# Kernel tuning notes

Hardware: AMD Instinct MI355X
Metric: run time of the kernel (lower is better)

The kernel has to match this reference:

```python
import jax, jax.numpy as jnp
import numpy as np
import math

B, N, D, H = 32, 577, 768, 12
HD = D // H  # 64
WS = 24  # window size
NUM_REL_DIST = (2 * WS - 1) * (2 * WS - 1) + 3  # 2212


def _build_rel_pos_index():
    ch, cw = np.arange(WS), np.arange(WS)
    coords = np.stack(np.meshgrid(ch, cw, indexing='ij'))  # [2, WS, WS]
    cf = coords.reshape(2, -1)  # [2, WS*WS]
    rel = cf[:, :, None] - cf[:, None, :]  # [2, WS*WS, WS*WS]
    rel = rel.transpose(1, 2, 0).astype(np.int64)
    rel[:, :, 0] += WS - 1
    rel[:, :, 1] += WS - 1
    rel[:, :, 0] *= 2 * WS - 1
    idx = np.zeros((WS * WS + 1, WS * WS + 1), dtype=np.int64)
    idx[1:, 1:] = rel.sum(-1)
    idx[0, 0:] = NUM_REL_DIST - 3
    idx[0:, 0] = NUM_REL_DIST - 2
    idx[0, 0] = NUM_REL_DIST - 1
    return idx.astype(np.int32)


def setup_inputs() -> dict:
    key = jax.random.key(0)
    ks = jax.random.split(key, 7)
    s = 1.0 / math.sqrt(D)
    return {
        'hidden_states': jax.random.normal(ks[0], (B, N, D), jnp.float32),
        'q_w': jax.random.normal(ks[1], (D, D), jnp.float32) * s,
        'q_b': jax.random.normal(ks[2], (D,), jnp.float32) * 0.02,
        'k_w': jax.random.normal(ks[3], (D, D), jnp.float32) * s,
        'v_w': jax.random.normal(ks[4], (D, D), jnp.float32) * s,
        'v_b': jax.random.normal(ks[5], (D,), jnp.float32) * 0.02,
        'rel_pos_table': jax.random.normal(ks[6], (NUM_REL_DIST, H), jnp.float32) * 0.02,
        'rel_pos_index': jnp.asarray(_build_rel_pos_index()),
    }


def reference(hidden_states, q_w, q_b, k_w, v_w, v_b, rel_pos_table, rel_pos_index):
    # QKV projections (torch Linear: x @ W.T + b); key has no bias
    q = hidden_states @ q_w.T + q_b  # [B,N,D]
    k = hidden_states @ k_w.T        # [B,N,D]
    v = hidden_states @ v_w.T + v_b  # [B,N,D]

    def heads(x):
        return x.reshape(B, N, H, HD).transpose(0, 2, 1, 3)  # [B,H,N,HD]

    q, k, v = heads(q), heads(k), heads(v)
    scores = jnp.einsum('bhqd,bhkd->bhqk', q, k) / math.sqrt(HD)
    # relative position bias: table lookup -> [N,N,H] -> [H,N,N]
    bias = rel_pos_table[rel_pos_index.reshape(-1)].reshape(N, N, H)
    scores = scores + bias.transpose(2, 0, 1)[None]
    probs = jax.nn.softmax(scores, axis=-1)  # dropout p=0 (eval)
    ctx = jnp.einsum('bhqk,bhkd->bhqd', probs, v)
    return ctx.transpose(0, 2, 1, 3).reshape(B, N, D)
```

## Files before the change

kernel.cpp:

```cpp
#include <hip/hip_runtime.h>
#include <hip/hip_bf16.h>

#define B_  32
#define N_  577
#define D_  768
#define H_  12
#define HD_ 64
#define M_  (B_ * N_)
#define NW_ (3 * D_)
#define VN_ 640
#define BPAD_ 640
#define SCALE_ 0.18033688f

typedef __bf16 bf16_t;
typedef __bf16 bf16x8 __attribute__((ext_vector_type(8)));
typedef __bf16 bf16x4 __attribute__((ext_vector_type(4)));
typedef float  f32x4  __attribute__((ext_vector_type(4)));

static __device__ __forceinline__ bf16x8 ldg8(const bf16_t* p) {
    return *reinterpret_cast<const bf16x8*>(p);
}

#define GLOAD_LDS16(g, l)                                                     \
    __builtin_amdgcn_global_load_lds(                                         \
        (const __attribute__((address_space(1))) void*)(g),                   \
        (__attribute__((address_space(3))) void*)(l), 16, 0, 0)

__global__ void cvt_f32_bf16(const float* __restrict__ src,
                             bf16_t* __restrict__ dst, int n4) {
    int i = blockIdx.x * blockDim.x + threadIdx.x;
    if (i < n4) {
        float4 f = reinterpret_cast<const float4*>(src)[i];
        bf16x4 o;
        o.x = (bf16_t)f.x; o.y = (bf16_t)f.y; o.z = (bf16_t)f.z; o.w = (bf16_t)f.w;
        *reinterpret_cast<bf16x4*>(dst + (size_t)i * 4) = o;
    }
}

__global__ void cvt3_f32_bf16(const float* __restrict__ s0,
                              const float* __restrict__ s1,
                              const float* __restrict__ s2,
                              bf16_t* __restrict__ dst, int n4) {
    int i = blockIdx.x * blockDim.x + threadIdx.x;
    if (i < n4) {
        const float* src = blockIdx.y == 0 ? s0 : (blockIdx.y == 1 ? s1 : s2);
        float4 f = reinterpret_cast<const float4*>(src)[i];
        bf16x4 o;
        o.x = (bf16_t)f.x; o.y = (bf16_t)f.y; o.z = (bf16_t)f.z; o.w = (bf16_t)f.w;
        *reinterpret_cast<bf16x4*>(dst + (size_t)blockIdx.y * n4 * 4 + (size_t)i * 4) = o;
    }
}

__global__ void build_bias_t(const float* __restrict__ table,
                             const int* __restrict__ idx,
                             float* __restrict__ biasT) {
    int col = blockIdx.x;
    int h   = blockIdx.y;
    float* dst = biasT + ((size_t)h * BPAD_ + col) * BPAD_;
    if (col < N_) {
        for (int row = threadIdx.x; row < BPAD_; row += blockDim.x) {
            int rr = row < N_ ? row : (N_ - 1);
            int id = idx[rr * N_ + col];
            dst[row] = table[id * H_ + h] * 1.44269504f;
        }
    } else {
        for (int row = threadIdx.x; row < BPAD_; row += blockDim.x)
            dst[row] = -1e30f;
    }
}

__global__ __launch_bounds__(256) void qkv_gemm(
    const bf16_t* __restrict__ hb, const bf16_t* __restrict__ W,
    const float* __restrict__ qb, const float* __restrict__ vb,
    bf16_t* __restrict__ Q, bf16_t* __restrict__ K, bf16_t* __restrict__ VT)
{
    __shared__ __align__(16) char lds[65536];

    int tid = threadIdx.x;
    int w  = tid >> 6, l = tid & 63;
    int lr = l & 15, lg = l >> 4;
    int wm = w & 1,  wn = w >> 1;

    int wg = blockIdx.x;
    int xcd = wg & 7, pos = wg >> 3;
    const int Q8 = 2610 / 8, R8 = 2610 % 8;
    int base = xcd < R8 ? xcd * (Q8 + 1) : R8 * (Q8 + 1) + (xcd - R8) * Q8;
    int wgid = base + pos;
    int bx = wgid / 18, y = wgid - bx * 18;
    int brow = bx * 128;
    int mat = y / 6, ysub = y - mat * 6;
    int cbase = ysub * 128;

    int srow = tid >> 3;
    int sslot = (tid & 7) ^ (srow & 7);
    const bf16_t* pa[4];
    const bf16_t* pb[4];
#pragma unroll
    for (int r = 0; r < 4; ++r) {
        int ra = brow + r * 32 + srow; ra = ra < M_ ? ra : (M_ - 1);
        pa[r] = hb + (size_t)ra * D_ + sslot * 8;
        pb[r] = W + (size_t)(y * 128 + r * 32 + srow) * D_ + sslot * 8;
    }

    auto stage = [&](int buf, int k) {
#pragma unroll
        for (int r = 0; r < 4; ++r) {
            GLOAD_LDS16(pa[r] + k, lds + buf * 16384 + r * 4096 + tid * 16);
            GLOAD_LDS16(pb[r] + k, lds + 32768 + buf * 16384 + r * 4096 + tid * 16);
        }
    };

    f32x4 acc[4][4] = {};
    stage(0, 0);
    int cur = 0;
    for (int t = 0; t < 12; ++t) {
        if (t < 11) {
            stage(cur ^ 1, (t + 1) * 64);
            asm volatile("s_waitcnt vmcnt(8)" ::: "memory");
        } else {
            asm volatile("s_waitcnt vmcnt(0)" ::: "memory");
        }
        __builtin_amdgcn_s_barrier();
        __builtin_amdgcn_sched_barrier(0);

        const char* pA = lds + cur * 16384;
        const char* pB = lds + 32768 + cur * 16384;
#pragma unroll
        for (int kk = 0; kk < 2; ++kk) {
            bf16x8 af[4];
#pragma unroll
            for (int m = 0; m < 4; ++m) {
                int row = wm * 64 + m * 16 + lr;
                af[m] = *reinterpret_cast<const bf16x8*>(
                    pA + row * 128 + (((kk * 4 + lg) ^ (lr & 7)) << 4));
            }
#pragma unroll
            for (int n = 0; n < 4; ++n) {
                int row = wn * 64 + n * 16 + lr;
                bf16x8 bfr = *reinterpret_cast<const bf16x8*>(
                    pB + row * 128 + (((kk * 4 + lg) ^ (lr & 7)) << 4));
#pragma unroll
                for (int m = 0; m < 4; ++m)
                    acc[m][n] = __builtin_amdgcn_mfma_f32_16x16x32_bf16(
                        af[m], bfr, acc[m][n], 0, 0, 0);
            }
        }
        __builtin_amdgcn_sched_barrier(0);
        __builtin_amdgcn_s_barrier();
        cur ^= 1;
    }

    bf16_t* ep = (bf16_t*)lds;
    if (mat < 2) {
#pragma unroll
        for (int m = 0; m < 4; ++m)
#pragma unroll
            for (int n = 0; n < 4; ++n) {
                int col = wn * 64 + n * 16 + lr;
#pragma unroll
                for (int j = 0; j < 4; ++j) {
                    int row = wm * 64 + m * 16 + lg * 4 + j;
                    float v = acc[m][n][j];
                    v = (mat == 0) ? (v + qb[cbase + col]) * SCALE_ : v;
                    ep[row * 132 + col] = (bf16_t)v;
                }
            }
        __syncthreads();
        bf16_t* dst0 = (mat == 0) ? Q : K;
#pragma unroll
        for (int k = 0; k < 8; ++k) {
            int c = k * 256 + tid;
            int row = c >> 4, cc = c & 15;
            int grow = brow + row;
            if (grow < M_) {
                int bb = grow / N_, nn = grow - bb * N_;
                int col0 = cc * 8;
                int hh = ysub * 2 + (col0 >> 6);
                int hd0 = col0 & 63;
                bf16x8 vc = *reinterpret_cast<const bf16x8*>(ep + row * 132 + col0);
                *reinterpret_cast<bf16x8*>(
                    dst0 + ((size_t)(bb * H_ + hh) * N_ + nn) * HD_ + hd0) = vc;
            }
        }
    } else {
#pragma unroll
        for (int m = 0; m < 4; ++m)
#pragma unroll
            for (int n = 0; n < 4; ++n) {
                int col = wn * 64 + n * 16 + lr;
                float badd = vb[cbase + col];
#pragma unroll
                for (int j = 0; j < 4; ++j) {
                    int row = wm * 64 + m * 16 + lg * 4 + j;
                    ep[col * 132 + row] = (bf16_t)(acc[m][n][j] + badd);
                }
            }
        __syncthreads();
#pragma unroll
        for (int k = 0; k < 8; ++k) {
            int c = k * 256 + tid;
            int col = c >> 4, rc = c & 15;
            int grow0 = brow + rc * 8;
            int hh = ysub * 2 + (col >> 6), hd = col & 63;
            int bb = grow0 / N_, nn0 = grow0 - bb * N_;
            if (nn0 + 8 <= N_ && grow0 + 8 <= M_) {
                *reinterpret_cast<bf16x8*>(
                    VT + ((size_t)(bb * H_ + hh) * HD_ + hd) * VN_ + nn0) =
                    *reinterpret_cast<const bf16x8*>(ep + col * 132 + rc * 8);
            } else {
                for (int jj = 0; jj < 8; ++jj) {
                    int grow = grow0 + jj;
                    if (grow >= M_) break;
                    int b2 = grow / N_, n2 = grow - b2 * N_;
                    VT[((size_t)(b2 * H_ + hh) * HD_ + hd) * VN_ + n2] =
                        ep[col * 132 + rc * 8 + jj];
                }
            }
        }
    }
}

__global__ __launch_bounds__(256) void attn(
    const bf16_t* __restrict__ Q, const bf16_t* __restrict__ K,
    const bf16_t* __restrict__ VT, const float* __restrict__ biasT,
    float* __restrict__ out)
{
    __shared__ __align__(16) char Kl[2][8192];
    __shared__ __align__(16) char Vl[2][8192];
    __shared__ __align__(16) char Pl[4][2048];

    int tid = threadIdx.x;
    int w = tid >> 6, l = tid & 63, lr = l & 15, lg = l >> 4;

    int wg = blockIdx.x;
    int wgid = (wg & 7) * 480 + (wg >> 3);
    int h = wgid / 320;
    int rem = wgid - h * 320;
    int b = rem / 10;
    int qt = rem - b * 10;

    const bf16_t* Qp = Q  + (size_t)(b * H_ + h) * N_ * HD_;
    const bf16_t* Kp = K  + (size_t)(b * H_ + h) * N_ * HD_;
    const bf16_t* Vp = VT + (size_t)(b * H_ + h) * HD_ * VN_;
    const float*  bp = biasT + (size_t)h * BPAD_ * BPAD_;

    int q0 = qt * 64 + w * 16;
    int qrow = q0 + lr;
    int qrow_c = qrow < N_ ? qrow : (N_ - 1);
    bf16x8 aQ0 = ldg8(Qp + (size_t)qrow_c * HD_ + lg * 8);
    bf16x8 aQ1 = ldg8(Qp + (size_t)qrow_c * HD_ + 32 + lg * 8);

    bf16x8 vone;
#pragma unroll
    for (int i = 0; i < 8; ++i) vone[i] = (bf16_t)1.0f;

    int rloc = l >> 3;
    int cswz = (l & 7) ^ rloc;
    const bf16_t* Kst[2];
    const bf16_t* Vst[2];
#pragma unroll
    for (int rnd = 0; rnd < 2; ++rnd) {
        int r = rnd * 32 + w * 8 + rloc;
        Kst[rnd] = Kp + (size_t)r * HD_ + cswz * 8;
        Vst[rnd] = Vp + (size_t)r * VN_ + cswz * 8;
    }

    f32x4 o[4] = {};
    f32x4 osum = {};
    char* Pw = Pl[w];
    const int NT = 10;

    auto stageKV = [&](int buf, int k0) {
#pragma unroll
        for (int rnd = 0; rnd < 2; ++rnd)
            GLOAD_LDS16(Kst[rnd] + (size_t)k0 * HD_,
                        Kl[buf] + rnd * 4096 + w * 1024);
#pragma unroll
        for (int rnd = 0; rnd < 2; ++rnd)
            GLOAD_LDS16(Vst[rnd] + k0, Vl[buf] + rnd * 4096 + w * 1024);
    };
    auto loadBias = [&](int k0, f32x4* bbv) {
#pragma unroll
        for (int kt = 0; kt < 4; ++kt)
            bbv[kt] = *reinterpret_cast<const f32x4*>(
                bp + (size_t)(k0 + kt * 16 + lr) * BPAD_ + q0 + lg * 4);
    };

    auto tile = [&](int t, int rbuf, const f32x4* bbcur, f32x4* bbnxt) {
        int k0 = t * 64;
        if (t + 1 < NT) {
            stageKV(rbuf ^ 1, k0 + 64);
            loadBias(k0 + 64, bbnxt);
        }
        __builtin_amdgcn_sched_barrier(0);

        f32x4 s[4];
        __builtin_amdgcn_s_setprio(1);
#pragma unroll
        for (int kt = 0; kt < 4; ++kt) {
            int r = kt * 16 + lr;
            bf16x8 kf0 = *reinterpret_cast<const bf16x8*>(
                Kl[rbuf] + r * 128 + ((lg ^ (r & 7)) << 4));
            bf16x8 kf1 = *reinterpret_cast<const bf16x8*>(
                Kl[rbuf] + r * 128 + (((4 + lg) ^ (r & 7)) << 4));
            f32x4 a = __builtin_amdgcn_mfma_f32_16x16x32_bf16(
                aQ0, kf0, bbcur[kt], 0, 0, 0);
            s[kt] = __builtin_amdgcn_mfma_f32_16x16x32_bf16(aQ1, kf1, a, 0, 0, 0);
        }
        __builtin_amdgcn_s_setprio(0);

#pragma unroll
        for (int kt = 0; kt < 4; ++kt)
#pragma unroll
            for (int j = 0; j < 4; ++j) {
                float p = __builtin_amdgcn_exp2f(s[kt][j]);
                int row = lg * 4 + j;
                int byte = (row * 128 + (kt * 16 + lr) * 2) ^ ((row & 7) << 4);
                *reinterpret_cast<bf16_t*>(Pw + byte) = (bf16_t)p;
            }

        __builtin_amdgcn_s_setprio(1);
#pragma unroll
        for (int kc = 0; kc < 2; ++kc) {
            int pbyte = (lr * 128 + kc * 64 + lg * 16) ^ ((lr & 7) << 4);
            bf16x8 aP = *reinterpret_cast<const bf16x8*>(Pw + pbyte);
            osum = __builtin_amdgcn_mfma_f32_16x16x32_bf16(aP, vone, osum, 0, 0, 0);
#pragma unroll
            for (int ft = 0; ft < 4; ++ft) {
                int d = ft * 16 + lr;
                bf16x8 bV = *reinterpret_cast<const bf16x8*>(
                    Vl[rbuf] + d * 128 + (((kc * 4 + lg) ^ (d & 7)) << 4));
                o[ft] = __builtin_amdgcn_mfma_f32_16x16x32_bf16(aP, bV, o[ft], 0, 0, 0);
            }
        }
        __builtin_amdgcn_s_setprio(0);
        __builtin_amdgcn_sched_barrier(0);

        if (t + 1 < NT) asm volatile("s_waitcnt vmcnt(4)" ::: "memory");
        else            asm volatile("s_waitcnt vmcnt(0)" ::: "memory");
        __builtin_amdgcn_s_barrier();
        __builtin_amdgcn_sched_barrier(0);
    };

    f32x4 bbA[4], bbB[4];
    stageKV(0, 0);
    loadBias(0, bbA);
    asm volatile("s_waitcnt vmcnt(4)" ::: "memory");
    __builtin_amdgcn_s_barrier();
    __builtin_amdgcn_sched_barrier(0);

    for (int tp = 0; tp < NT / 2; ++tp) {
        tile(tp * 2,     0, bbA, bbB);
        tile(tp * 2 + 1, 1, bbB, bbA);
    }

#pragma unroll
    for (int j = 0; j < 4; ++j) {
        int row = q0 + lg * 4 + j;
        if (row < N_) {
            float inv = 1.f / osum[j];
#pragma unroll
            for (int ft = 0; ft < 4; ++ft)
                out[((size_t)(b * N_ + row)) * D_ + h * HD_ + ft * 16 + lr] =
                    o[ft][j] * inv;
        }
    }
}

extern "C" void kernel_launch(void* const* d_in, const int* in_sizes, int n_in,
                              void* d_out, int out_size, void* d_ws, size_t ws_size,
                              hipStream_t stream)
{
    const float* hs    = (const float*)d_in[0];
    const float* q_w   = (const float*)d_in[1];
    const float* q_b   = (const float*)d_in[2];
    const float* k_w   = (const float*)d_in[3];
    const float* v_w   = (const float*)d_in[4];
    const float* v_b   = (const float*)d_in[5];
    const float* table = (const float*)d_in[6];
    const int*   rpi   = (const int*)d_in[7];
    float* out = (float*)d_out;

    char* ws = (char*)d_ws;
    size_t off = 0;
    auto alloc = [&](size_t bytes) {
        char* p = ws + off;
        off = (off + bytes + 255) & ~(size_t)255;
        return p;
    };
    bf16_t* hb  = (bf16_t*)alloc((size_t)M_ * D_ * 2);
    bf16_t* Wc  = (bf16_t*)alloc((size_t)NW_ * D_ * 2);
    bf16_t* Qb  = (bf16_t*)alloc((size_t)B_ * H_ * N_ * HD_ * 2);
    bf16_t* Kb  = (bf16_t*)alloc((size_t)B_ * H_ * N_ * HD_ * 2 + 16384);
    bf16_t* VTb = (bf16_t*)alloc((size_t)B_ * H_ * HD_ * VN_ * 2);
    float*  bia = (float*)alloc((size_t)H_ * BPAD_ * BPAD_ * 4);

    int n4h = M_ * D_ / 4;
    cvt_f32_bf16<<<(n4h + 255) / 256, 256, 0, stream>>>(hs, hb, n4h);
    int n4w = D_ * D_ / 4;
    cvt3_f32_bf16<<<dim3((n4w + 255) / 256, 3), 256, 0, stream>>>(
        q_w, k_w, v_w, Wc, n4w);
    build_bias_t<<<dim3(BPAD_, H_), 256, 0, stream>>>(table, rpi, bia);

    qkv_gemm<<<2610, 256, 0, stream>>>(hb, Wc, q_b, v_b, Qb, Kb, VTb);

    attn<<<3840, 256, 0, stream>>>(Qb, Kb, VTb, bia, out);
}
```

Before: 238.4 us.

## Process two 64-query tiles per attention workgroup to reuse staged K/V

Each attention workgroup now computes 128 query rows (two 16-row sub-tiles per wave) against the same K/V tiles staged in LDS, halving the grid size. This is meant to halve K/V global loads and LDS staging per query and give each wave more independent MFMA work. In exchange it doubles accumulator and bias registers per thread, which may reduce occupancy, and leaves fewer workgroups to balance across CUs.

```diff
diff --git a/kernel.cpp b/kernel.cpp
--- a/kernel.cpp
+++ b/kernel.cpp
@@ -227,28 +227,34 @@
 {
     __shared__ __align__(16) char Kl[2][8192];
     __shared__ __align__(16) char Vl[2][8192];
-    __shared__ __align__(16) char Pl[4][2048];
+    __shared__ __align__(16) char Pl[4][2][2048];
 
     int tid = threadIdx.x;
     int w = tid >> 6, l = tid & 63, lr = l & 15, lg = l >> 4;
 
     int wg = blockIdx.x;
-    int wgid = (wg & 7) * 480 + (wg >> 3);
-    int h = wgid / 320;
-    int rem = wgid - h * 320;
-    int b = rem / 10;
-    int qt = rem - b * 10;
+    int wgid = (wg & 7) * 240 + (wg >> 3);
+    int h = wgid / 160;
+    int rem = wgid - h * 160;
+    int b = rem / 5;
+    int qt = rem - b * 5;
 
     const bf16_t* Qp = Q  + (size_t)(b * H_ + h) * N_ * HD_;
     const bf16_t* Kp = K  + (size_t)(b * H_ + h) * N_ * HD_;
     const bf16_t* Vp = VT + (size_t)(b * H_ + h) * HD_ * VN_;
     const float*  bp = biasT + (size_t)h * BPAD_ * BPAD_;
 
-    int q0 = qt * 64 + w * 16;
-    int qrow = q0 + lr;
-    int qrow_c = qrow < N_ ? qrow : (N_ - 1);
-    bf16x8 aQ0 = ldg8(Qp + (size_t)qrow_c * HD_ + lg * 8);
-    bf16x8 aQ1 = ldg8(Qp + (size_t)qrow_c * HD_ + 32 + lg * 8);
+    int q0A = qt * 128 + w * 16;
+    int q0B = q0A + 64;
+    bf16x8 aQ0A, aQ1A, aQ0B, aQ1B;
+    {
+        int qa = q0A + lr; qa = qa < N_ ? qa : (N_ - 1);
+        int qb2 = q0B + lr; qb2 = qb2 < N_ ? qb2 : (N_ - 1);
+        aQ0A = ldg8(Qp + (size_t)qa * HD_ + lg * 8);
+        aQ1A = ldg8(Qp + (size_t)qa * HD_ + 32 + lg * 8);
+        aQ0B = ldg8(Qp + (size_t)qb2 * HD_ + lg * 8);
+        aQ1B = ldg8(Qp + (size_t)qb2 * HD_ + 32 + lg * 8);
+    }
 
     bf16x8 vone;
 #pragma unroll
@@ -265,9 +271,10 @@
         Vst[rnd] = Vp + (size_t)r * VN_ + cswz * 8;
     }
 
-    f32x4 o[4] = {};
-    f32x4 osum = {};
-    char* Pw = Pl[w];
+    f32x4 oA[4] = {}, oB[4] = {};
+    f32x4 osumA = {}, osumB = {};
+    char* PwA = Pl[w][0];
+    char* PwB = Pl[w][1];
     const int NT = 10;
 
     auto stageKV = [&](int buf, int k0) {
@@ -279,22 +286,25 @@
         for (int rnd = 0; rnd < 2; ++rnd)
             GLOAD_LDS16(Vst[rnd] + k0, Vl[buf] + rnd * 4096 + w * 1024);
     };
-    auto loadBias = [&](int k0, f32x4* bbv) {
-#pragma unroll
-        for (int kt = 0; kt < 4; ++kt)
-            bbv[kt] = *reinterpret_cast<const f32x4*>(
-                bp + (size_t)(k0 + kt * 16 + lr) * BPAD_ + q0 + lg * 4);
+    auto loadBias = [&](int k0, f32x4* bA, f32x4* bB) {
+#pragma unroll
+        for (int kt = 0; kt < 4; ++kt) {
+            const float* bcol = bp + (size_t)(k0 + kt * 16 + lr) * BPAD_;
+            bA[kt] = *reinterpret_cast<const f32x4*>(bcol + q0A + lg * 4);
+            bB[kt] = *reinterpret_cast<const f32x4*>(bcol + q0B + lg * 4);
+        }
     };
 
-    auto tile = [&](int t, int rbuf, const f32x4* bbcur, f32x4* bbnxt) {
+    auto tile = [&](int t, int rbuf, const f32x4* bcA, const f32x4* bcB,
+                    f32x4* bnA, f32x4* bnB) {
         int k0 = t * 64;
         if (t + 1 < NT) {
             stageKV(rbuf ^ 1, k0 + 64);
-            loadBias(k0 + 64, bbnxt);
+            loadBias(k0 + 64, bnA, bnB);
         }
         __builtin_amdgcn_sched_barrier(0);
 
-        f32x4 s[4];
+        f32x4 sA[4], sB[4];
         __builtin_amdgcn_s_setprio(1);
 #pragma unroll
         for (int kt = 0; kt < 4; ++kt) {
@@ -303,9 +313,12 @@
                 Kl[rbuf] + r * 128 + ((lg ^ (r & 7)) << 4));
             bf16x8 kf1 = *reinterpret_cast<const bf16x8*>(
                 Kl[rbuf] + r * 128 + (((4 + lg) ^ (r & 7)) << 4));
-            f32x4 a = __builtin_amdgcn_mfma_f32_16x16x32_bf16(
-                aQ0, kf0, bbcur[kt], 0, 0, 0);
-            s[kt] = __builtin_amdgcn_mfma_f32_16x16x32_bf16(aQ1, kf1, a, 0, 0, 0);
+            f32x4 a0 = __builtin_amdgcn_mfma_f32_16x16x32_bf16(
+                aQ0A, kf0, bcA[kt], 0, 0, 0);
+            sA[kt] = __builtin_amdgcn_mfma_f32_16x16x32_bf16(aQ1A, kf1, a0, 0, 0, 0);
+            f32x4 a1 = __builtin_amdgcn_mfma_f32_16x16x32_bf16(
+                aQ0B, kf0, bcB[kt], 0, 0, 0);
+            sB[kt] = __builtin_amdgcn_mfma_f32_16x16x32_bf16(aQ1B, kf1, a1, 0, 0, 0);
         }
         __builtin_amdgcn_s_setprio(0);
 
@@ -313,56 +326,69 @@
         for (int kt = 0; kt < 4; ++kt)
 #pragma unroll
             for (int j = 0; j < 4; ++j) {
-                float p = __builtin_amdgcn_exp2f(s[kt][j]);
                 int row = lg * 4 + j;
                 int byte = (row * 128 + (kt * 16 + lr) * 2) ^ ((row & 7) << 4);
-                *reinterpret_cast<bf16_t*>(Pw + byte) = (bf16_t)p;
+                *reinterpret_cast<bf16_t*>(PwA + byte) =
+                    (bf16_t)__builtin_amdgcn_exp2f(sA[kt][j]);
+                *reinterpret_cast<bf16_t*>(PwB + byte) =
+                    (bf16_t)__builtin_amdgcn_exp2f(sB[kt][j]);
             }
 
         __builtin_amdgcn_s_setprio(1);
 #pragma unroll
         for (int kc = 0; kc < 2; ++kc) {
             int pbyte = (lr * 128 + kc * 64 + lg * 16) ^ ((lr & 7) << 4);
-            bf16x8 aP = *reinterpret_cast<const bf16x8*>(Pw + pbyte);
-            osum = __builtin_amdgcn_mfma_f32_16x16x32_bf16(aP, vone, osum, 0, 0, 0);
+            bf16x8 aPA = *reinterpret_cast<const bf16x8*>(PwA + pbyte);
+            bf16x8 aPB = *reinterpret_cast<const bf16x8*>(PwB + pbyte);
+            osumA = __builtin_amdgcn_mfma_f32_16x16x32_bf16(aPA, vone, osumA, 0, 0, 0);
+            osumB = __builtin_amdgcn_mfma_f32_16x16x32_bf16(aPB, vone, osumB, 0, 0, 0);
 #pragma unroll
             for (int ft = 0; ft < 4; ++ft) {
                 int d = ft * 16 + lr;
                 bf16x8 bV = *reinterpret_cast<const bf16x8*>(
                     Vl[rbuf] + d * 128 + (((kc * 4 + lg) ^ (d & 7)) << 4));
-                o[ft] = __builtin_amdgcn_mfma_f32_16x16x32_bf16(aP, bV, o[ft], 0, 0, 0);
+                oA[ft] = __builtin_amdgcn_mfma_f32_16x16x32_bf16(aPA, bV, oA[ft], 0, 0, 0);
+                oB[ft] = __builtin_amdgcn_mfma_f32_16x16x32_bf16(aPB, bV, oB[ft], 0, 0, 0);
             }
         }
         __builtin_amdgcn_s_setprio(0);
         __builtin_amdgcn_sched_barrier(0);
 
-        if (t + 1 < NT) asm volatile("s_waitcnt vmcnt(4)" ::: "memory");
+        if (t + 1 < NT) asm volatile("s_waitcnt vmcnt(8)" ::: "memory");
         else            asm volatile("s_waitcnt vmcnt(0)" ::: "memory");
         __builtin_amdgcn_s_barrier();
         __builtin_amdgcn_sched_barrier(0);
     };
 
-    f32x4 bbA[4], bbB[4];
+    f32x4 bbA0[4], bbB0[4], bbA1[4], bbB1[4];
     stageKV(0, 0);
-    loadBias(0, bbA);
-    asm volatile("s_waitcnt vmcnt(4)" ::: "memory");
+    loadBias(0, bbA0, bbB0);
+    asm volatile("s_waitcnt vmcnt(8)" ::: "memory");
     __builtin_amdgcn_s_barrier();
     __builtin_amdgcn_sched_barrier(0);
 
     for (int tp = 0; tp < NT / 2; ++tp) {
-        tile(tp * 2,     0, bbA, bbB);
-        tile(tp * 2 + 1, 1, bbB, bbA);
+        tile(tp * 2,     0, bbA0, bbB0, bbA1, bbB1);
+        tile(tp * 2 + 1, 1, bbA1, bbB1, bbA0, bbB0);
     }
 
 #pragma unroll
     for (int j = 0; j < 4; ++j) {
-        int row = q0 + lg * 4 + j;
-        if (row < N_) {
-            float inv = 1.f / osum[j];
+        int rowA = q0A + lg * 4 + j;
+        if (rowA < N_) {
+            float inv = 1.f / osumA[j];
 #pragma unroll
             for (int ft = 0; ft < 4; ++ft)
-                out[((size_t)(b * N_ + row)) * D_ + h * HD_ + ft * 16 + lr] =
-                    o[ft][j] * inv;
+                out[((size_t)(b * N_ + rowA)) * D_ + h * HD_ + ft * 16 + lr] =
+                    oA[ft][j] * inv;
+        }
+        int rowB = q0B + lg * 4 + j;
+        if (rowB < N_) {
+            float inv = 1.f / osumB[j];
+#pragma unroll
+            for (int ft = 0; ft < 4; ++ft)
+                out[((size_t)(b * N_ + rowB)) * D_ + h * HD_ + ft * 16 + lr] =
+                    oB[ft][j] * inv;
         }
     }
 }
@@ -404,5 +430,5 @@
 
     qkv_gemm<<<2610, 256, 0, stream>>>(hb, Wc, q_b, v_b, Qb, Kb, VTb);
 
-    attn<<<3840, 256, 0, stream>>>(Qb, Kb, VTb, bia, out);
-}
+    attn<<<1920, 256, 0, stream>>>(Qb, Kb, VTb, bia, out);
+}
```

Result: slower. 308.5 us (+29.4%).
